# Performance work log

Hardware: AMD Instinct MI355X
Metric: run time of the kernel (lower is better)

Reference implementation:

```python
import jax, jax.numpy as jnp
import numpy as np

D = 512
H = 8
DH = D // H
SPK = 4
HG = 128  # max(16, D//4)
EPS = 1e-5


def _layernorm(x, gamma, beta):
    mu = jnp.mean(x, axis=-1, keepdims=True)
    var = jnp.var(x, axis=-1, keepdims=True)
    return (x - mu) * jax.lax.rsqrt(var + EPS) * gamma + beta


def setup_inputs() -> dict:
    key = jax.random.key(0)
    ks = jax.random.split(key, 16)
    B, T = 8, 4096
    s = 0.02
    return {
        'token_emb': jax.random.normal(ks[0], (B, T, D), jnp.float32),
        'speaker_emb': jax.random.normal(ks[1], (B, D), jnp.float32),
        'We': jax.random.normal(ks[2], (D * SPK, D), jnp.float32) * s,
        'be': jnp.zeros((D * SPK,), jnp.float32),
        'spk_pos': jax.random.normal(ks[3], (1, SPK, D), jnp.float32) * s,
        'Wq': jax.random.normal(ks[4], (D, D), jnp.float32) * s,
        'bq': jnp.zeros((D,), jnp.float32),
        'Wk': jax.random.normal(ks[5], (D, D), jnp.float32) * s,
        'bk': jnp.zeros((D,), jnp.float32),
        'Wv': jax.random.normal(ks[6], (D, D), jnp.float32) * s,
        'bv': jnp.zeros((D,), jnp.float32),
        'Wo': jax.random.normal(ks[7], (D, D), jnp.float32) * s,
        'bo': jnp.zeros((D,), jnp.float32),
        'gln_gamma': jnp.ones((D,), jnp.float32),
        'gln_beta': jnp.zeros((D,), jnp.float32),
        'Wg1': jax.random.normal(ks[8], (HG, D), jnp.float32) * s,
        'bg1': jnp.zeros((HG,), jnp.float32),
        'Wg2': jax.random.normal(ks[9], (1, HG), jnp.float32) * s,
        'bg2': jnp.zeros((1,), jnp.float32),
        'ln_gamma': jnp.ones((D,), jnp.float32),
        'ln_beta': jnp.zeros((D,), jnp.float32),
    }


def reference(token_emb, speaker_emb, We, be, spk_pos, Wq, bq, Wk, bk, Wv, bv,
              Wo, bo, gln_gamma, gln_beta, Wg1, bg1, Wg2, bg2, ln_gamma, ln_beta):
    B, T, _ = token_emb.shape
    # speaker expansion: (B,D) -> (B, SPK*D) -> (B,SPK,D), plus learned pos
    spk_tokens = jax.nn.relu(speaker_emb @ We.T + be).reshape(B, SPK, D) + spk_pos
    # multi-head cross-attention (batch_first, eval-mode dropout = identity)
    q = (token_emb @ Wq.T + bq).reshape(B, T, H, DH)
    k = (spk_tokens @ Wk.T + bk).reshape(B, SPK, H, DH)
    v = (spk_tokens @ Wv.T + bv).reshape(B, SPK, H, DH)
    scores = jnp.einsum('bthd,bshd->bhts', q, k) / jnp.sqrt(jnp.float32(DH))
    w = jax.nn.softmax(scores, axis=-1)  # (B,H,T,SPK)
    ctx = jnp.einsum('bhts,bshd->bthd', w, v).reshape(B, T, D)
    attn_output = ctx @ Wo.T + bo
    attn_weights = jnp.mean(w, axis=1)  # torch MHA averages heads -> (B,T,SPK)
    # gate: LN -> Linear -> ReLU -> Linear -> Sigmoid
    g = _layernorm(token_emb, gln_gamma, gln_beta)
    g = jax.nn.relu(g @ Wg1.T + bg1)
    g_used = jax.nn.sigmoid(g @ Wg2.T + bg2)  # (B,T,1)
    # residual + final LayerNorm (dropout identity in eval)
    fused = _layernorm(token_emb + g_used * attn_output, ln_gamma, ln_beta)
    return (fused, attn_weights, g_used)
```

## Files before the change

### kernel.cpp

```cpp
#include <hip/hip_runtime.h>
#include <hip/hip_bf16.h>
#include <stdint.h>

typedef __attribute__((ext_vector_type(8))) short short8;
typedef __attribute__((ext_vector_type(4))) short short4v;
typedef __attribute__((ext_vector_type(4))) float f32x4;
typedef __attribute__((ext_vector_type(2))) unsigned int uint2v;

#define DD 512
#define TT 16
#define TN 4096
#define NB 8

__device__ __forceinline__ unsigned short f2bf(float f){
  uint32_t u = __float_as_uint(f);
  u += 0x7FFFu + ((u >> 16) & 1u);
  return (unsigned short)(u >> 16);
}
__device__ __forceinline__ float bf2f(unsigned short h){
  return __uint_as_float(((uint32_t)h) << 16);
}


__global__ void prep_spk(const float* __restrict__ se, const float* __restrict__ We,
                         const float* __restrict__ be, const float* __restrict__ spos,
                         float* __restrict__ spk){
  int idx = blockIdx.x * 256 + threadIdx.x;
  int sub = idx & 15; int out = idx >> 4;
  int b = out & 7, od = out >> 3;
  const float* wr = We + (size_t)od * DD + sub * 4;
  const float* sb = se + b * DD + sub * 4;
  float acc = 0.f;
#pragma unroll
  for (int i = 0; i < 8; i++){
    float4 w = *(const float4*)(wr + i * 64);
    float4 x = *(const float4*)(sb + i * 64);
    acc += w.x * x.x + w.y * x.y + w.z * x.z + w.w * x.w;
  }
  acc += __shfl_xor(acc, 1); acc += __shfl_xor(acc, 2);
  acc += __shfl_xor(acc, 4); acc += __shfl_xor(acc, 8);
  if (sub == 0) spk[b * 2048 + od] = fmaxf(acc + be[od], 0.f) + spos[od];
}

__global__ void prep_kv(const float* __restrict__ spk, const float* __restrict__ Wk,
                        const float* __restrict__ bk, const float* __restrict__ Wv,
                        const float* __restrict__ bv, float* __restrict__ kb,
                        float* __restrict__ vb){
  int idx = blockIdx.x * 256 + threadIdx.x;
  int sub = idx & 15; int out = idx >> 4;
  int hd = out >> 5; int r = out & 31; int b = r >> 2, s = r & 3;
  const float* sp  = spk + (b * 4 + s) * DD + sub * 4;
  const float* wkr = Wk + (size_t)hd * DD + sub * 4;
  const float* wvr = Wv + (size_t)hd * DD + sub * 4;
  float ak = 0.f, av = 0.f;
#pragma unroll
  for (int i = 0; i < 8; i++){
    float4 x  = *(const float4*)(sp + i * 64);
    float4 wk = *(const float4*)(wkr + i * 64);
    float4 wv = *(const float4*)(wvr + i * 64);
    ak += x.x * wk.x + x.y * wk.y + x.z * wk.z + x.w * wk.w;
    av += x.x * wv.x + x.y * wv.y + x.z * wv.z + x.w * wv.w;
  }
  ak += __shfl_xor(ak, 1); ak += __shfl_xor(ak, 2);
  ak += __shfl_xor(ak, 4); ak += __shfl_xor(ak, 8);
  av += __shfl_xor(av, 1); av += __shfl_xor(av, 2);
  av += __shfl_xor(av, 4); av += __shfl_xor(av, 8);
  if (sub == 0){
    kb[(b * 4 + s) * DD + hd] = ak + bk[hd];
    vb[(b * 4 + s) * DD + hd] = av + bv[hd];
  }
}

__global__ void prep_mu(const float* __restrict__ kb, const float* __restrict__ vb,
                        const float* __restrict__ Wq, const float* __restrict__ bq,
                        const float* __restrict__ Wo, const float* __restrict__ bo,
                        const float* __restrict__ Wg1,
                        const float* __restrict__ glng, const float* __restrict__ glnb,
                        const float* __restrict__ bg1,
                        unsigned short* __restrict__ mS, unsigned short* __restrict__ uS,
                        float* __restrict__ cArr, unsigned short* __restrict__ wg1S,
                        float* __restrict__ e1, float* __restrict__ e2){
  int idx = blockIdx.x * 256 + threadIdx.x;
  if (idx < 131072){
    int d = idx & 511; int j = (idx >> 9) & 31; int b = idx >> 14;
    int h = j >> 2, s = j & 3;
    const float* kr = kb + (b * 4 + s) * DD + h * 64;
    const float* wq = Wq + (size_t)(h * 64) * DD + d;
    float acc = 0.f;
#pragma unroll 16
    for (int dh = 0; dh < 64; dh++) acc += wq[(size_t)dh * DD] * kr[dh];
    int kt = d >> 5, kgp = (d >> 3) & 3, e = d & 7;
    int half = j >> 4;
    mS[(size_t)(b * 16 + kt) * 1024 + half * 512 + (kgp * 16 + (j & 15)) * 8 + e] = f2bf(acc);
  } else if (idx < 262144){
    int t = idx - 131072;
    int j = t & 31; int d = (t >> 5) & 511; int b = t >> 14;
    int h = j >> 2, s = j & 3;
    const float* vr = vb + (b * 4 + s) * DD + h * 64;
    const float* wo = Wo + (size_t)d * DD + h * 64;
    float acc = 0.f;
#pragma unroll 8
    for (int dh = 0; dh < 64; dh += 4){
      float4 v4 = *(const float4*)(vr + dh);
      float4 w4 = *(const float4*)(wo + dh);
      acc += v4.x * w4.x + v4.y * w4.y + v4.z * w4.z + v4.w * w4.w;
    }
    int nc = d >> 7, nt = (d >> 4) & 7, r16p = d & 15;
    int kgp = j >> 3, e = j & 7;
    uS[(size_t)(b * 32 + nc * 8 + nt) * 512 + (kgp * 16 + r16p) * 8 + e] =
        f2bf(acc + bo[d] * 0.125f);
  } else if (idx < 327680){
    int t = idx - 262144;
    int col = t >> 9, d = t & 511;
    int nt = col >> 4, c16 = col & 15;
    int kt = d >> 5, kgp = (d >> 3) & 3, e = d & 7;
    wg1S[(size_t)(nt * 16 + kt) * 512 + (kgp * 16 + c16) * 8 + e] = f2bf(Wg1[t] * glng[d]);
  } else if (idx < 327936){
    int t = idx - 327680; int j = t & 31, b = t >> 5;
    int h = j >> 2, s = j & 3;
    const float* kr = kb + (b * 4 + s) * DD + h * 64;
    const float* bqp = bq + h * 64;
    float acc = 0.f;
    for (int dh = 0; dh < 64; dh++) acc += bqp[dh] * kr[dh];
    cArr[b * 32 + j] = acc;
  } else if (idx < 328064){
    int col = idx - 327936;
    const float* wr = Wg1 + (size_t)col * DD;
    float a1 = 0.f, a2 = 0.f;
    for (int d = 0; d < DD; d += 4){
      float4 w  = *(const float4*)(wr + d);
      float4 gm = *(const float4*)(glng + d);
      float4 bt = *(const float4*)(glnb + d);
      a1 += w.x * gm.x + w.y * gm.y + w.z * gm.z + w.w * gm.w;
      a2 += w.x * bt.x + w.y * bt.y + w.z * bt.z + w.w * bt.w;
    }
    e1[col] = a1; e2[col] = a2 + bg1[col];
  }
}


__global__ __launch_bounds__(256, 4) void fused_main(
    const float* __restrict__ xin,
    const float* __restrict__ e1v, const float* __restrict__ e2v,
    const float* __restrict__ wg2v, const float* __restrict__ bg2v,
    const float* __restrict__ lng, const float* __restrict__ lnb,
    const unsigned short* __restrict__ mS,
    const unsigned short* __restrict__ uS,
    const float* __restrict__ cArr,
    const unsigned short* __restrict__ wg1S,
    float* __restrict__ outF, float* __restrict__ outAW, float* __restrict__ outG)
{
  __shared__ __align__(16) unsigned short Yb[TT * DD];
  __shared__ __align__(16) unsigned short Wl[TT * 32];
  __shared__ float smu[TT], srs[TT];
  __shared__ float aws[2][64];
  __shared__ float gp[4][TT];
  __shared__ float pp[4][TT], qq[4][TT];

  const int tid  = threadIdx.x;
  const int w    = tid >> 6;
  const int lane = tid & 63;
  const int r16  = lane & 15;
  const int kg   = lane >> 4;
  const int bb   = blockIdx.x >> 8;
  const int t0   = (blockIdx.x & 255) << 4;
  const size_t rowbase = (size_t)bb * TN + t0;
  const int swzS = (r16 & 7) << 3;

  const float* xbase = xin + rowbase * DD;
#pragma unroll
  for (int i = 0; i < 4; ++i){
    const int rr = w * 4 + i;
    const int swz = (rr & 7) << 3;
    float s = 0.f, q = 0.f;
#pragma unroll
    for (int h2 = 0; h2 < 2; ++h2){
      const int col = h2 * 256 + lane * 4;
      float4 v4 = *(const float4*)(xbase + rr * DD + col);
      float xv[4] = {v4.x, v4.y, v4.z, v4.w};
      short4v pk;
#pragma unroll
      for (int j = 0; j < 4; ++j){ s += xv[j]; q += xv[j]*xv[j]; pk[j] = (short)f2bf(xv[j]); }
      *(short4v*)&Yb[rr * DD + (col ^ swz)] = pk;
    }
#pragma unroll
    for (int off = 1; off < 64; off <<= 1){ s += __shfl_xor(s, off); q += __shfl_xor(q, off); }
    if (lane == 0){
      const float mu = s * (1.f/DD);
      smu[rr] = mu;
      srs[rr] = rsqrtf(q * (1.f/DD) - mu*mu + 1e-5f);
    }
  }
  __syncthreads();

  const int half = w & 1;
  const int nt0 = w * 2;
  const unsigned short* mSp  = mS + (size_t)bb * 16384 + half * 512 + lane * 8;
  const unsigned short* wgp0 = wg1S + (size_t)(nt0 * 16) * 512 + lane * 8;
  const unsigned short* wgp1 = wgp0 + (size_t)16 * 512;
  f32x4 sa = {0.f,0.f,0.f,0.f}, ga0 = {0.f,0.f,0.f,0.f}, ga1 = {0.f,0.f,0.f,0.f};
  if (w < 2){
#pragma unroll
    for (int kt = 0; kt < 16; ++kt){
      short8 af = *(const short8*)&Yb[r16 * DD + ((kt*32 + kg*8) ^ swzS)];
      short8 b0 = *(const short8*)(mSp + (size_t)kt * 1024);
      sa  = __builtin_amdgcn_mfma_f32_16x16x32_bf16(af, b0, sa, 0, 0, 0);
      short8 wf0 = *(const short8*)(wgp0 + (size_t)kt * 512);
      ga0 = __builtin_amdgcn_mfma_f32_16x16x32_bf16(wf0, af, ga0, 0, 0, 0);
      short8 wf1 = *(const short8*)(wgp1 + (size_t)kt * 512);
      ga1 = __builtin_amdgcn_mfma_f32_16x16x32_bf16(wf1, af, ga1, 0, 0, 0);
    }
  } else {
#pragma unroll
    for (int kt = 0; kt < 16; ++kt){
      short8 af = *(const short8*)&Yb[r16 * DD + ((kt*32 + kg*8) ^ swzS)];
      short8 wf0 = *(const short8*)(wgp0 + (size_t)kt * 512);
      ga0 = __builtin_amdgcn_mfma_f32_16x16x32_bf16(wf0, af, ga0, 0, 0, 0);
      short8 wf1 = *(const short8*)(wgp1 + (size_t)kt * 512);
      ga1 = __builtin_amdgcn_mfma_f32_16x16x32_bf16(wf1, af, ga1, 0, 0, 0);
    }
  }

  float4 e1c[2], e2c[2], w2c[2];
#pragma unroll
  for (int t = 0; t < 2; ++t){
    const int c4 = (nt0 + t) * 16 + kg * 4;
    e1c[t] = *(const float4*)(e1v + c4);
    e2c[t] = *(const float4*)(e2v + c4);
    w2c[t] = *(const float4*)(wg2v + c4);
  }
  float4 lgh[2], lbh[2];
#pragma unroll
  for (int h2 = 0; h2 < 2; ++h2){
    lgh[h2] = *(const float4*)(lng + h2*256 + lane*4);
    lbh[h2] = *(const float4*)(lnb + h2*256 + lane*4);
  }
  const float bg2s = bg2v[0];

  if (w < 2){
    const float cv = cArr[bb*32 + half*16 + r16];
#pragma unroll
    for (int r = 0; r < 4; ++r){
      float s0 = (sa[r] + cv) * 0.125f;
      float mx = fmaxf(s0, __shfl_xor(s0, 1)); mx = fmaxf(mx, __shfl_xor(mx, 2));
      float e0 = __expf(s0 - mx);
      float d0 = e0; d0 += __shfl_xor(d0, 1); d0 += __shfl_xor(d0, 2);
      float wv = e0 / d0;
      float t = wv; t += __shfl_xor(t, 4); t += __shfl_xor(t, 8);
      const int rw = kg * 4 + r;
      Wl[rw * 32 + half * 16 + r16] = f2bf(wv);
      if ((lane & 12) == 0) aws[half][rw * 4 + (lane & 3)] = t;
    }
  }

  {
    const float mu_t = smu[r16], rs_t = srs[r16];
    float part = 0.f;
#pragma unroll
    for (int t = 0; t < 2; ++t){
      const f32x4 ga = t ? ga1 : ga0;
      float ea[4] = {e1c[t].x, e1c[t].y, e1c[t].z, e1c[t].w};
      float eb[4] = {e2c[t].x, e2c[t].y, e2c[t].z, e2c[t].w};
      float wc[4] = {w2c[t].x, w2c[t].y, w2c[t].z, w2c[t].w};
#pragma unroll
      for (int r = 0; r < 4; ++r){
        float gv = rs_t * (ga[r] - mu_t * ea[r]) + eb[r];
        part += fmaxf(gv, 0.f) * wc[r];
      }
    }
    part += __shfl_xor(part, 16); part += __shfl_xor(part, 32);
    if (kg == 0) gp[w][r16] = part;
  }
  __syncthreads();

  if (w == 2){
    const int tok = lane >> 2;
    const float val = (aws[0][lane] + aws[1][lane]) * 0.125f;
    outAW[(rowbase + tok) * 4 + (lane & 3)] = val;
  }
  float g_reg;
  {
    const float gs = gp[0][r16] + gp[1][r16] + gp[2][r16] + gp[3][r16];
    g_reg = 1.f / (1.f + __expf(-(gs + bg2s)));
    if (w == 3 && kg == 0) outG[rowbase + r16] = g_reg;
  }

  short8 awf = *(const short8*)&Wl[r16 * 32 + kg * 8];
  const unsigned short* uSp = uS + (size_t)bb * 16384 + (size_t)(w * 8) * 512 + lane * 8;
  f32x4 acc[8];
#pragma unroll
  for (int nt = 0; nt < 8; ++nt){
    short8 uf = *(const short8*)(uSp + (size_t)nt * 512);
    f32x4 z = {0.f,0.f,0.f,0.f};
    acc[nt] = __builtin_amdgcn_mfma_f32_16x16x32_bf16(uf, awf, z, 0, 0, 0);
  }
  float psum = 0.f, psq = 0.f;
#pragma unroll
  for (int nt = 0; nt < 8; ++nt){
    const int c4 = w * 128 + nt * 16 + kg * 4;
    const int idx = r16 * DD + (c4 ^ swzS);
    uint2v xch = *(const uint2v*)&Yb[idx];
    unsigned int lo = xch[0], hi = xch[1];
    float y0 = bf2f((unsigned short)(lo & 0xffffu)) + g_reg * acc[nt][0];
    float y1 = bf2f((unsigned short)(lo >> 16))     + g_reg * acc[nt][1];
    float y2 = bf2f((unsigned short)(hi & 0xffffu)) + g_reg * acc[nt][2];
    float y3 = bf2f((unsigned short)(hi >> 16))     + g_reg * acc[nt][3];
    psum += (y0 + y1) + (y2 + y3);
    psq  += (y0*y0 + y1*y1) + (y2*y2 + y3*y3);
    uint2v yp;
    yp[0] = (unsigned)f2bf(y0) | ((unsigned)f2bf(y1) << 16);
    yp[1] = (unsigned)f2bf(y2) | ((unsigned)f2bf(y3) << 16);
    *(uint2v*)&Yb[idx] = yp;
  }
  psum += __shfl_xor(psum, 16); psum += __shfl_xor(psum, 32);
  psq  += __shfl_xor(psq, 16);  psq  += __shfl_xor(psq, 32);
  if (kg == 0){ pp[w][r16] = psum; qq[w][r16] = psq; }
  __syncthreads();

#pragma unroll
  for (int i = 0; i < 4; ++i){
    const int rr = w * 4 + i;
    const float sm = pp[0][rr] + pp[1][rr] + pp[2][rr] + pp[3][rr];
    const float sq = qq[0][rr] + qq[1][rr] + qq[2][rr] + qq[3][rr];
    const float mu2 = sm * (1.f/DD);
    const float rs2 = rsqrtf(sq * (1.f/DD) - mu2*mu2 + 1e-5f);
    const int swz = (rr & 7) << 3;
#pragma unroll
    for (int h2 = 0; h2 < 2; ++h2){
      const int col = h2 * 256 + lane * 4;
      short4v yv = *(const short4v*)&Yb[rr * DD + (col ^ swz)];
      float la[4] = {lgh[h2].x, lgh[h2].y, lgh[h2].z, lgh[h2].w};
      float lb4[4] = {lbh[h2].x, lbh[h2].y, lbh[h2].z, lbh[h2].w};
      float4 o;
      o.x = (bf2f((unsigned short)yv[0]) - mu2) * rs2 * la[0] + lb4[0];
      o.y = (bf2f((unsigned short)yv[1]) - mu2) * rs2 * la[1] + lb4[1];
      o.z = (bf2f((unsigned short)yv[2]) - mu2) * rs2 * la[2] + lb4[2];
      o.w = (bf2f((unsigned short)yv[3]) - mu2) * rs2 * la[3] + lb4[3];
      *(float4*)(outF + (rowbase + rr) * DD + col) = o;
    }
  }
}


extern "C" void kernel_launch(void* const* d_in, const int* in_sizes, int n_in,
                              void* d_out, int out_size, void* d_ws, size_t ws_size,
                              hipStream_t stream)
{
  const float* token = (const float*)d_in[0];
  const float* semb  = (const float*)d_in[1];
  const float* We    = (const float*)d_in[2];
  const float* be    = (const float*)d_in[3];
  const float* spos  = (const float*)d_in[4];
  const float* Wq    = (const float*)d_in[5];
  const float* bq    = (const float*)d_in[6];
  const float* Wk    = (const float*)d_in[7];
  const float* bk    = (const float*)d_in[8];
  const float* Wv    = (const float*)d_in[9];
  const float* bv    = (const float*)d_in[10];
  const float* Wo    = (const float*)d_in[11];
  const float* bo    = (const float*)d_in[12];
  const float* glng  = (const float*)d_in[13];
  const float* glnb  = (const float*)d_in[14];
  const float* Wg1   = (const float*)d_in[15];
  const float* bg1   = (const float*)d_in[16];
  const float* Wg2   = (const float*)d_in[17];
  const float* bg2   = (const float*)d_in[18];
  const float* lng   = (const float*)d_in[19];
  const float* lnb   = (const float*)d_in[20];

  char* ws = (char*)d_ws;
  float* e1             = (float*)(ws + 0);
  float* e2             = (float*)(ws + 512);
  float* spk            = (float*)(ws + 0);
  float* kb             = (float*)(ws + 65536);
  float* vb             = (float*)(ws + 131072);
  unsigned short* mS    = (unsigned short*)(ws + 196608);
  unsigned short* uS    = (unsigned short*)(ws + 458752);
  float* cArr           = (float*)(ws + 720896);
  unsigned short* wg1S  = (unsigned short*)(ws + 721920);

  float* outF  = (float*)d_out;
  float* outAW = outF + (size_t)NB * TN * DD;
  float* outG  = outAW + (size_t)NB * TN * 4;

  prep_spk<<<dim3(1024), dim3(256), 0, stream>>>(semb, We, be, spos, spk);
  prep_kv<<<dim3(1024), dim3(256), 0, stream>>>(spk, Wk, bk, Wv, bv, kb, vb);
  prep_mu<<<dim3(1282), dim3(256), 0, stream>>>(kb, vb, Wq, bq, Wo, bo, Wg1, glng, glnb, bg1,
                                                mS, uS, cArr, wg1S, e1, e2);
  fused_main<<<dim3(NB * TN / TT), dim3(256), 0, stream>>>(
      token, e1, e2, Wg2, bg2, lng, lnb,
      mS, uS, cArr, wg1S, outF, outAW, outG);
}
```

Baseline: 68.51 us.

## Process 64 tokens per block and batch prep kernels for weight reuse

```diff
diff --git a/kernel.cpp b/kernel.cpp
--- a/kernel.cpp
+++ b/kernel.cpp
@@ -8,7 +8,7 @@
 typedef __attribute__((ext_vector_type(2))) unsigned int uint2v;
 
 #define DD 512
-#define TT 16
+#define TT 64
 #define TN 4096
 #define NB 8
 
@@ -26,20 +26,29 @@
                          const float* __restrict__ be, const float* __restrict__ spos,
                          float* __restrict__ spk){
   int idx = blockIdx.x * 256 + threadIdx.x;
-  int sub = idx & 15; int out = idx >> 4;
-  int b = out & 7, od = out >> 3;
-  const float* wr = We + (size_t)od * DD + sub * 4;
-  const float* sb = se + b * DD + sub * 4;
-  float acc = 0.f;
-#pragma unroll
-  for (int i = 0; i < 8; i++){
-    float4 w = *(const float4*)(wr + i * 64);
-    float4 x = *(const float4*)(sb + i * 64);
-    acc += w.x * x.x + w.y * x.y + w.z * x.z + w.w * x.w;
-  }
-  acc += __shfl_xor(acc, 1); acc += __shfl_xor(acc, 2);
-  acc += __shfl_xor(acc, 4); acc += __shfl_xor(acc, 8);
-  if (sub == 0) spk[b * 2048 + od] = fmaxf(acc + be[od], 0.f) + spos[od];
+  int sub = idx & 15, od = idx >> 4;
+  const float* wr = We + (size_t)od * DD + sub * 32;
+  float acc[8] = {0.f,0.f,0.f,0.f,0.f,0.f,0.f,0.f};
+#pragma unroll
+  for (int i = 0; i < 8; ++i){
+    float4 w4 = *(const float4*)(wr + i * 4);
+#pragma unroll
+    for (int b = 0; b < 8; ++b){
+      float4 s4 = *(const float4*)(se + b * DD + sub * 32 + i * 4);
+      acc[b] += w4.x*s4.x + w4.y*s4.y + w4.z*s4.z + w4.w*s4.w;
+    }
+  }
+#pragma unroll
+  for (int b = 0; b < 8; ++b){
+    acc[b] += __shfl_xor(acc[b], 1); acc[b] += __shfl_xor(acc[b], 2);
+    acc[b] += __shfl_xor(acc[b], 4); acc[b] += __shfl_xor(acc[b], 8);
+  }
+  if (sub == 0){
+    const float bev = be[od], sp = spos[od];
+#pragma unroll
+    for (int b = 0; b < 8; ++b)
+      spk[b * 2048 + od] = fmaxf(acc[b] + bev, 0.f) + sp;
+  }
 }
 
 __global__ void prep_kv(const float* __restrict__ spk, const float* __restrict__ Wk,
@@ -47,27 +56,35 @@
                         const float* __restrict__ bv, float* __restrict__ kb,
                         float* __restrict__ vb){
   int idx = blockIdx.x * 256 + threadIdx.x;
-  int sub = idx & 15; int out = idx >> 4;
-  int hd = out >> 5; int r = out & 31; int b = r >> 2, s = r & 3;
-  const float* sp  = spk + (b * 4 + s) * DD + sub * 4;
-  const float* wkr = Wk + (size_t)hd * DD + sub * 4;
-  const float* wvr = Wv + (size_t)hd * DD + sub * 4;
-  float ak = 0.f, av = 0.f;
-#pragma unroll
-  for (int i = 0; i < 8; i++){
-    float4 x  = *(const float4*)(sp + i * 64);
-    float4 wk = *(const float4*)(wkr + i * 64);
-    float4 wv = *(const float4*)(wvr + i * 64);
-    ak += x.x * wk.x + x.y * wk.y + x.z * wk.z + x.w * wk.w;
-    av += x.x * wv.x + x.y * wv.y + x.z * wv.z + x.w * wv.w;
-  }
-  ak += __shfl_xor(ak, 1); ak += __shfl_xor(ak, 2);
-  ak += __shfl_xor(ak, 4); ak += __shfl_xor(ak, 8);
-  av += __shfl_xor(av, 1); av += __shfl_xor(av, 2);
-  av += __shfl_xor(av, 4); av += __shfl_xor(av, 8);
+  int sub = idx & 15, hd = (idx >> 4) & 511, b = idx >> 13;
+  const float* wkr = Wk + (size_t)hd * DD + sub * 32;
+  const float* wvr = Wv + (size_t)hd * DD + sub * 32;
+  float aK[4] = {0.f,0.f,0.f,0.f}, aV[4] = {0.f,0.f,0.f,0.f};
+#pragma unroll
+  for (int i = 0; i < 8; ++i){
+    float4 wk4 = *(const float4*)(wkr + i * 4);
+    float4 wv4 = *(const float4*)(wvr + i * 4);
+#pragma unroll
+    for (int s = 0; s < 4; ++s){
+      float4 x4 = *(const float4*)(spk + (b * 4 + s) * DD + sub * 32 + i * 4);
+      aK[s] += x4.x*wk4.x + x4.y*wk4.y + x4.z*wk4.z + x4.w*wk4.w;
+      aV[s] += x4.x*wv4.x + x4.y*wv4.y + x4.z*wv4.z + x4.w*wv4.w;
+    }
+  }
+#pragma unroll
+  for (int s = 0; s < 4; ++s){
+    aK[s] += __shfl_xor(aK[s], 1); aK[s] += __shfl_xor(aK[s], 2);
+    aK[s] += __shfl_xor(aK[s], 4); aK[s] += __shfl_xor(aK[s], 8);
+    aV[s] += __shfl_xor(aV[s], 1); aV[s] += __shfl_xor(aV[s], 2);
+    aV[s] += __shfl_xor(aV[s], 4); aV[s] += __shfl_xor(aV[s], 8);
+  }
   if (sub == 0){
-    kb[(b * 4 + s) * DD + hd] = ak + bk[hd];
-    vb[(b * 4 + s) * DD + hd] = av + bv[hd];
+    const float bkv = bk[hd], bvv = bv[hd];
+#pragma unroll
+    for (int s = 0; s < 4; ++s){
+      kb[(b * 4 + s) * DD + hd] = aK[s] + bkv;
+      vb[(b * 4 + s) * DD + hd] = aV[s] + bvv;
+    }
   }
 }
 
@@ -81,19 +98,29 @@
                         float* __restrict__ cArr, unsigned short* __restrict__ wg1S,
                         float* __restrict__ e1, float* __restrict__ e2){
   int idx = blockIdx.x * 256 + threadIdx.x;
-  if (idx < 131072){
-    int d = idx & 511; int j = (idx >> 9) & 31; int b = idx >> 14;
+  if (idx < 32768){
+    int dc = idx & 127, j = (idx >> 7) & 31, b = idx >> 12;
     int h = j >> 2, s = j & 3;
+    const int d0 = dc * 4;
     const float* kr = kb + (b * 4 + s) * DD + h * 64;
-    const float* wq = Wq + (size_t)(h * 64) * DD + d;
-    float acc = 0.f;
-#pragma unroll 16
-    for (int dh = 0; dh < 64; dh++) acc += wq[(size_t)dh * DD] * kr[dh];
-    int kt = d >> 5, kgp = (d >> 3) & 3, e = d & 7;
-    int half = j >> 4;
-    mS[(size_t)(b * 16 + kt) * 1024 + half * 512 + (kgp * 16 + (j & 15)) * 8 + e] = f2bf(acc);
-  } else if (idx < 262144){
-    int t = idx - 131072;
+    const float* wqb = Wq + (size_t)(h * 64) * DD + d0;
+    float4 acc = {0.f, 0.f, 0.f, 0.f};
+#pragma unroll 8
+    for (int dh = 0; dh < 64; ++dh){
+      float4 w4 = *(const float4*)(wqb + (size_t)dh * DD);
+      float kvv = kr[dh];
+      acc.x += kvv * w4.x; acc.y += kvv * w4.y;
+      acc.z += kvv * w4.z; acc.w += kvv * w4.w;
+    }
+    const int kt = d0 >> 5, kgp = (d0 >> 3) & 3, e0 = d0 & 7, half = j >> 4;
+    unsigned short* dst = mS + (size_t)(b * 16 + kt) * 1024 + half * 512 +
+                          (kgp * 16 + (j & 15)) * 8 + e0;
+    short4v st;
+    st[0] = (short)f2bf(acc.x); st[1] = (short)f2bf(acc.y);
+    st[2] = (short)f2bf(acc.z); st[3] = (short)f2bf(acc.w);
+    *(short4v*)dst = st;
+  } else if (idx < 163840){
+    int t = idx - 32768;
     int j = t & 31; int d = (t >> 5) & 511; int b = t >> 14;
     int h = j >> 2, s = j & 3;
     const float* vr = vb + (b * 4 + s) * DD + h * 64;
@@ -109,22 +136,22 @@
     int kgp = j >> 3, e = j & 7;
     uS[(size_t)(b * 32 + nc * 8 + nt) * 512 + (kgp * 16 + r16p) * 8 + e] =
         f2bf(acc + bo[d] * 0.125f);
-  } else if (idx < 327680){
-    int t = idx - 262144;
+  } else if (idx < 229376){
+    int t = idx - 163840;
     int col = t >> 9, d = t & 511;
     int nt = col >> 4, c16 = col & 15;
     int kt = d >> 5, kgp = (d >> 3) & 3, e = d & 7;
     wg1S[(size_t)(nt * 16 + kt) * 512 + (kgp * 16 + c16) * 8 + e] = f2bf(Wg1[t] * glng[d]);
-  } else if (idx < 327936){
-    int t = idx - 327680; int j = t & 31, b = t >> 5;
+  } else if (idx < 229632){
+    int t = idx - 229376; int j = t & 31, b = t >> 5;
     int h = j >> 2, s = j & 3;
     const float* kr = kb + (b * 4 + s) * DD + h * 64;
     const float* bqp = bq + h * 64;
     float acc = 0.f;
     for (int dh = 0; dh < 64; dh++) acc += bqp[dh] * kr[dh];
     cArr[b * 32 + j] = acc;
-  } else if (idx < 328064){
-    int col = idx - 327936;
+  } else if (idx < 229760){
+    int col = idx - 229632;
     const float* wr = Wg1 + (size_t)col * DD;
     float a1 = 0.f, a2 = 0.f;
     for (int d = 0; d < DD; d += 4){
@@ -139,7 +166,7 @@
 }
 
 
-__global__ __launch_bounds__(256, 4) void fused_main(
+__global__ __launch_bounds__(256, 2) void fused_main(
     const float* __restrict__ xin,
     const float* __restrict__ e1v, const float* __restrict__ e2v,
     const float* __restrict__ wg2v, const float* __restrict__ bg2v,
@@ -153,7 +180,7 @@
   __shared__ __align__(16) unsigned short Yb[TT * DD];
   __shared__ __align__(16) unsigned short Wl[TT * 32];
   __shared__ float smu[TT], srs[TT];
-  __shared__ float aws[2][64];
+  __shared__ float aws[2][TT * 4];
   __shared__ float gp[4][TT];
   __shared__ float pp[4][TT], qq[4][TT];
 
@@ -162,25 +189,26 @@
   const int lane = tid & 63;
   const int r16  = lane & 15;
   const int kg   = lane >> 4;
-  const int bb   = blockIdx.x >> 8;
-  const int t0   = (blockIdx.x & 255) << 4;
+  const int bb   = blockIdx.x >> 6;
+  const int t0   = (blockIdx.x & 63) << 6;
   const size_t rowbase = (size_t)bb * TN + t0;
   const int swzS = (r16 & 7) << 3;
 
   const float* xbase = xin + rowbase * DD;
 #pragma unroll
-  for (int i = 0; i < 4; ++i){
-    const int rr = w * 4 + i;
+  for (int i = 0; i < 16; ++i){
+    const int rr = w * 16 + i;
     const int swz = (rr & 7) << 3;
     float s = 0.f, q = 0.f;
 #pragma unroll
     for (int h2 = 0; h2 < 2; ++h2){
       const int col = h2 * 256 + lane * 4;
       float4 v4 = *(const float4*)(xbase + rr * DD + col);
-      float xv[4] = {v4.x, v4.y, v4.z, v4.w};
       short4v pk;
-#pragma unroll
-      for (int j = 0; j < 4; ++j){ s += xv[j]; q += xv[j]*xv[j]; pk[j] = (short)f2bf(xv[j]); }
+      pk[0] = (short)f2bf(v4.x); pk[1] = (short)f2bf(v4.y);
+      pk[2] = (short)f2bf(v4.z); pk[3] = (short)f2bf(v4.w);
+      s += (v4.x + v4.y) + (v4.z + v4.w);
+      q += (v4.x*v4.x + v4.y*v4.y) + (v4.z*v4.z + v4.w*v4.w);
       *(short4v*)&Yb[rr * DD + (col ^ swz)] = pk;
     }
 #pragma unroll
@@ -194,31 +222,43 @@
   __syncthreads();
 
   const int half = w & 1;
-  const int nt0 = w * 2;
+  const int sr0  = w >> 1;
+  const int sc0row = sr0 * 16 + r16;
+  const int sc1row = sc0row + 32;
+  const int nt0  = w * 2;
   const unsigned short* mSp  = mS + (size_t)bb * 16384 + half * 512 + lane * 8;
   const unsigned short* wgp0 = wg1S + (size_t)(nt0 * 16) * 512 + lane * 8;
   const unsigned short* wgp1 = wgp0 + (size_t)16 * 512;
-  f32x4 sa = {0.f,0.f,0.f,0.f}, ga0 = {0.f,0.f,0.f,0.f}, ga1 = {0.f,0.f,0.f,0.f};
-  if (w < 2){
-#pragma unroll
-    for (int kt = 0; kt < 16; ++kt){
-      short8 af = *(const short8*)&Yb[r16 * DD + ((kt*32 + kg*8) ^ swzS)];
-      short8 b0 = *(const short8*)(mSp + (size_t)kt * 1024);
-      sa  = __builtin_amdgcn_mfma_f32_16x16x32_bf16(af, b0, sa, 0, 0, 0);
-      short8 wf0 = *(const short8*)(wgp0 + (size_t)kt * 512);
-      ga0 = __builtin_amdgcn_mfma_f32_16x16x32_bf16(wf0, af, ga0, 0, 0, 0);
-      short8 wf1 = *(const short8*)(wgp1 + (size_t)kt * 512);
-      ga1 = __builtin_amdgcn_mfma_f32_16x16x32_bf16(wf1, af, ga1, 0, 0, 0);
-    }
-  } else {
-#pragma unroll
-    for (int kt = 0; kt < 16; ++kt){
-      short8 af = *(const short8*)&Yb[r16 * DD + ((kt*32 + kg*8) ^ swzS)];
-      short8 wf0 = *(const short8*)(wgp0 + (size_t)kt * 512);
-      ga0 = __builtin_amdgcn_mfma_f32_16x16x32_bf16(wf0, af, ga0, 0, 0, 0);
-      short8 wf1 = *(const short8*)(wgp1 + (size_t)kt * 512);
-      ga1 = __builtin_amdgcn_mfma_f32_16x16x32_bf16(wf1, af, ga1, 0, 0, 0);
-    }
+
+  f32x4 sa0 = {0.f,0.f,0.f,0.f}, sa1 = {0.f,0.f,0.f,0.f};
+  f32x4 gacc[2][4];
+#pragma unroll
+  for (int t = 0; t < 2; ++t)
+#pragma unroll
+    for (int rg = 0; rg < 4; ++rg){ f32x4 z = {0.f,0.f,0.f,0.f}; gacc[t][rg] = z; }
+
+#pragma unroll
+  for (int kt = 0; kt < 16; ++kt){
+    const int cofs = (kt * 32 + kg * 8) ^ swzS;
+    short8 af0 = *(const short8*)&Yb[( 0 + r16) * DD + cofs];
+    short8 af1 = *(const short8*)&Yb[(16 + r16) * DD + cofs];
+    short8 af2 = *(const short8*)&Yb[(32 + r16) * DD + cofs];
+    short8 af3 = *(const short8*)&Yb[(48 + r16) * DD + cofs];
+    short8 asc0 = *(const short8*)&Yb[sc0row * DD + cofs];
+    short8 asc1 = *(const short8*)&Yb[sc1row * DD + cofs];
+    short8 bm = *(const short8*)(mSp + (size_t)kt * 1024);
+    sa0 = __builtin_amdgcn_mfma_f32_16x16x32_bf16(asc0, bm, sa0, 0, 0, 0);
+    sa1 = __builtin_amdgcn_mfma_f32_16x16x32_bf16(asc1, bm, sa1, 0, 0, 0);
+    short8 wf0 = *(const short8*)(wgp0 + (size_t)kt * 512);
+    short8 wf1 = *(const short8*)(wgp1 + (size_t)kt * 512);
+    gacc[0][0] = __builtin_amdgcn_mfma_f32_16x16x32_bf16(wf0, af0, gacc[0][0], 0, 0, 0);
+    gacc[0][1] = __builtin_amdgcn_mfma_f32_16x16x32_bf16(wf0, af1, gacc[0][1], 0, 0, 0);
+    gacc[0][2] = __builtin_amdgcn_mfma_f32_16x16x32_bf16(wf0, af2, gacc[0][2], 0, 0, 0);
+    gacc[0][3] = __builtin_amdgcn_mfma_f32_16x16x32_bf16(wf0, af3, gacc[0][3], 0, 0, 0);
+    gacc[1][0] = __builtin_amdgcn_mfma_f32_16x16x32_bf16(wf1, af0, gacc[1][0], 0, 0, 0);
+    gacc[1][1] = __builtin_amdgcn_mfma_f32_16x16x32_bf16(wf1, af1, gacc[1][1], 0, 0, 0);
+    gacc[1][2] = __builtin_amdgcn_mfma_f32_16x16x32_bf16(wf1, af2, gacc[1][2], 0, 0, 0);
+    gacc[1][3] = __builtin_amdgcn_mfma_f32_16x16x32_bf16(wf1, af3, gacc[1][3], 0, 0, 0);
   }
 
   float4 e1c[2], e2c[2], w2c[2];
@@ -237,89 +277,104 @@
   }
   const float bg2s = bg2v[0];
 
-  if (w < 2){
+  {
     const float cv = cArr[bb*32 + half*16 + r16];
 #pragma unroll
-    for (int r = 0; r < 4; ++r){
-      float s0 = (sa[r] + cv) * 0.125f;
-      float mx = fmaxf(s0, __shfl_xor(s0, 1)); mx = fmaxf(mx, __shfl_xor(mx, 2));
-      float e0 = __expf(s0 - mx);
-      float d0 = e0; d0 += __shfl_xor(d0, 1); d0 += __shfl_xor(d0, 2);
-      float wv = e0 / d0;
-      float t = wv; t += __shfl_xor(t, 4); t += __shfl_xor(t, 8);
-      const int rw = kg * 4 + r;
-      Wl[rw * 32 + half * 16 + r16] = f2bf(wv);
-      if ((lane & 12) == 0) aws[half][rw * 4 + (lane & 3)] = t;
-    }
-  }
-
-  {
-    const float mu_t = smu[r16], rs_t = srs[r16];
+    for (int t2 = 0; t2 < 2; ++t2){
+      const f32x4 sa = t2 ? sa1 : sa0;
+      const int rgbase = (t2 ? (sr0 + 2) : sr0) * 16;
+#pragma unroll
+      for (int r = 0; r < 4; ++r){
+        float s0 = (sa[r] + cv) * 0.125f;
+        float mx = fmaxf(s0, __shfl_xor(s0, 1)); mx = fmaxf(mx, __shfl_xor(mx, 2));
+        float e0 = __expf(s0 - mx);
+        float d0 = e0; d0 += __shfl_xor(d0, 1); d0 += __shfl_xor(d0, 2);
+        float wv = e0 / d0;
+        float tt = wv; tt += __shfl_xor(tt, 4); tt += __shfl_xor(tt, 8);
+        const int rw = rgbase + kg * 4 + r;
+        Wl[rw * 32 + half * 16 + r16] = f2bf(wv);
+        if ((lane & 12) == 0) aws[half][rw * 4 + (lane & 3)] = tt;
+      }
+    }
+  }
+
+#pragma unroll
+  for (int rg = 0; rg < 4; ++rg){
+    const float mu_t = smu[rg*16 + r16], rs_t = srs[rg*16 + r16];
     float part = 0.f;
 #pragma unroll
     for (int t = 0; t < 2; ++t){
-      const f32x4 ga = t ? ga1 : ga0;
       float ea[4] = {e1c[t].x, e1c[t].y, e1c[t].z, e1c[t].w};
       float eb[4] = {e2c[t].x, e2c[t].y, e2c[t].z, e2c[t].w};
       float wc[4] = {w2c[t].x, w2c[t].y, w2c[t].z, w2c[t].w};
 #pragma unroll
       for (int r = 0; r < 4; ++r){
-        float gv = rs_t * (ga[r] - mu_t * ea[r]) + eb[r];
+        float gv = rs_t * (gacc[t][rg][r] - mu_t * ea[r]) + eb[r];
         part += fmaxf(gv, 0.f) * wc[r];
       }
     }
     part += __shfl_xor(part, 16); part += __shfl_xor(part, 32);
-    if (kg == 0) gp[w][r16] = part;
+    if (kg == 0) gp[w][rg*16 + r16] = part;
   }
   __syncthreads();
 
-  if (w == 2){
-    const int tok = lane >> 2;
-    const float val = (aws[0][lane] + aws[1][lane]) * 0.125f;
-    outAW[(rowbase + tok) * 4 + (lane & 3)] = val;
-  }
-  float g_reg;
   {
-    const float gs = gp[0][r16] + gp[1][r16] + gp[2][r16] + gp[3][r16];
-    g_reg = 1.f / (1.f + __expf(-(gs + bg2s)));
-    if (w == 3 && kg == 0) outG[rowbase + r16] = g_reg;
-  }
-
-  short8 awf = *(const short8*)&Wl[r16 * 32 + kg * 8];
+    const int tok = w * 16 + (lane >> 2);
+    const int si = lane & 3;
+    const float val = (aws[0][tok*4 + si] + aws[1][tok*4 + si]) * 0.125f;
+    outAW[(rowbase + tok) * 4 + si] = val;
+  }
+
+  float g_loc[4];
+#pragma unroll
+  for (int rg = 0; rg < 4; ++rg){
+    const int tk = rg*16 + r16;
+    const float gs = gp[0][tk] + gp[1][tk] + gp[2][tk] + gp[3][tk];
+    g_loc[rg] = 1.f / (1.f + __expf(-(gs + bg2s)));
+    if (rg == w && kg == 0) outG[rowbase + tk] = g_loc[rg];
+  }
+
   const unsigned short* uSp = uS + (size_t)bb * 16384 + (size_t)(w * 8) * 512 + lane * 8;
-  f32x4 acc[8];
-#pragma unroll
-  for (int nt = 0; nt < 8; ++nt){
-    short8 uf = *(const short8*)(uSp + (size_t)nt * 512);
-    f32x4 z = {0.f,0.f,0.f,0.f};
-    acc[nt] = __builtin_amdgcn_mfma_f32_16x16x32_bf16(uf, awf, z, 0, 0, 0);
-  }
-  float psum = 0.f, psq = 0.f;
-#pragma unroll
-  for (int nt = 0; nt < 8; ++nt){
-    const int c4 = w * 128 + nt * 16 + kg * 4;
-    const int idx = r16 * DD + (c4 ^ swzS);
-    uint2v xch = *(const uint2v*)&Yb[idx];
-    unsigned int lo = xch[0], hi = xch[1];
-    float y0 = bf2f((unsigned short)(lo & 0xffffu)) + g_reg * acc[nt][0];
-    float y1 = bf2f((unsigned short)(lo >> 16))     + g_reg * acc[nt][1];
-    float y2 = bf2f((unsigned short)(hi & 0xffffu)) + g_reg * acc[nt][2];
-    float y3 = bf2f((unsigned short)(hi >> 16))     + g_reg * acc[nt][3];
-    psum += (y0 + y1) + (y2 + y3);
-    psq  += (y0*y0 + y1*y1) + (y2*y2 + y3*y3);
-    uint2v yp;
-    yp[0] = (unsigned)f2bf(y0) | ((unsigned)f2bf(y1) << 16);
-    yp[1] = (unsigned)f2bf(y2) | ((unsigned)f2bf(y3) << 16);
-    *(uint2v*)&Yb[idx] = yp;
-  }
-  psum += __shfl_xor(psum, 16); psum += __shfl_xor(psum, 32);
-  psq  += __shfl_xor(psq, 16);  psq  += __shfl_xor(psq, 32);
-  if (kg == 0){ pp[w][r16] = psum; qq[w][r16] = psq; }
+  short8 uf[8];
+#pragma unroll
+  for (int nt = 0; nt < 8; ++nt) uf[nt] = *(const short8*)(uSp + (size_t)nt * 512);
+
+#pragma unroll
+  for (int rg = 0; rg < 4; ++rg){
+    short8 awf = *(const short8*)&Wl[(rg*16 + r16) * 32 + kg * 8];
+    f32x4 acc[8];
+#pragma unroll
+    for (int nt = 0; nt < 8; ++nt){
+      f32x4 z = {0.f,0.f,0.f,0.f};
+      acc[nt] = __builtin_amdgcn_mfma_f32_16x16x32_bf16(uf[nt], awf, z, 0, 0, 0);
+    }
+    float psum = 0.f, psq = 0.f;
+#pragma unroll
+    for (int nt = 0; nt < 8; ++nt){
+      const int c4 = w * 128 + nt * 16 + kg * 4;
+      const int idx = (rg*16 + r16) * DD + (c4 ^ swzS);
+      uint2v xch = *(const uint2v*)&Yb[idx];
+      unsigned int lo = xch[0], hi = xch[1];
+      float y0 = bf2f((unsigned short)(lo & 0xffffu)) + g_loc[rg] * acc[nt][0];
+      float y1 = bf2f((unsigned short)(lo >> 16))     + g_loc[rg] * acc[nt][1];
+      float y2 = bf2f((unsigned short)(hi & 0xffffu)) + g_loc[rg] * acc[nt][2];
+      float y3 = bf2f((unsigned short)(hi >> 16))     + g_loc[rg] * acc[nt][3];
+      psum += (y0 + y1) + (y2 + y3);
+      psq  += (y0*y0 + y1*y1) + (y2*y2 + y3*y3);
+      uint2v yp;
+      yp[0] = (unsigned)f2bf(y0) | ((unsigned)f2bf(y1) << 16);
+      yp[1] = (unsigned)f2bf(y2) | ((unsigned)f2bf(y3) << 16);
+      *(uint2v*)&Yb[idx] = yp;
+    }
+    psum += __shfl_xor(psum, 16); psum += __shfl_xor(psum, 32);
+    psq  += __shfl_xor(psq, 16);  psq  += __shfl_xor(psq, 32);
+    if (kg == 0){ pp[w][rg*16 + r16] = psum; qq[w][rg*16 + r16] = psq; }
+  }
   __syncthreads();
 
 #pragma unroll
-  for (int i = 0; i < 4; ++i){
-    const int rr = w * 4 + i;
+  for (int i = 0; i < 16; ++i){
+    const int rr = w * 16 + i;
     const float sm = pp[0][rr] + pp[1][rr] + pp[2][rr] + pp[3][rr];
     const float sq = qq[0][rr] + qq[1][rr] + qq[2][rr] + qq[3][rr];
     const float mu2 = sm * (1.f/DD);
@@ -383,10 +438,10 @@
   float* outAW = outF + (size_t)NB * TN * DD;
   float* outG  = outAW + (size_t)NB * TN * 4;
 
-  prep_spk<<<dim3(1024), dim3(256), 0, stream>>>(semb, We, be, spos, spk);
-  prep_kv<<<dim3(1024), dim3(256), 0, stream>>>(spk, Wk, bk, Wv, bv, kb, vb);
-  prep_mu<<<dim3(1282), dim3(256), 0, stream>>>(kb, vb, Wq, bq, Wo, bo, Wg1, glng, glnb, bg1,
-                                                mS, uS, cArr, wg1S, e1, e2);
+  prep_spk<<<dim3(128), dim3(256), 0, stream>>>(semb, We, be, spos, spk);
+  prep_kv<<<dim3(256), dim3(256), 0, stream>>>(spk, Wk, bk, Wv, bv, kb, vb);
+  prep_mu<<<dim3(898), dim3(256), 0, stream>>>(kb, vb, Wq, bq, Wo, bo, Wg1, glng, glnb, bg1,
+                                               mS, uS, cArr, wg1S, e1, e2);
   fused_main<<<dim3(NB * TN / TT), dim3(256), 0, stream>>>(
       token, e1, e2, Wg2, bg2, lng, lnb,
       mS, uS, cArr, wg1S, outF, outAW, outG);
```

Result: slower. 80.49 us (+17.5%).
